# Performance work log

Measured on AMD Instinct MI355X. Metric: run time of the kernel, lower is better.

Reference implementation:

```python
import jax, jax.numpy as jnp
import numpy as np

B, S, DIM = 2, 2048, 2048
H = 16
KV_RANK = 512
D_NOPE, D_ROPE, D_V = 128, 64, 128
QK_HEAD = D_NOPE + D_ROPE  # 192
THETA = 10000.0


def make_freqs(seqlen, d_rope, theta=THETA):
    inv = 1.0 / (theta ** (np.arange(0, d_rope, 2, dtype=np.float32) / d_rope))
    ang = np.outer(np.arange(seqlen, dtype=np.float32), inv)  # [S, d/2]
    return jnp.asarray(np.cos(ang)), jnp.asarray(np.sin(ang))


def apply_rope(x, cos, sin):
    # x: [b, s, h, d]; cos/sin: [s, d//2]; complex-pair rotation (interleaved pairs)
    xr = x.reshape(*x.shape[:-1], -1, 2)
    re, im = xr[..., 0], xr[..., 1]
    c = cos[None, :, None, :]
    s = sin[None, :, None, :]
    out = jnp.stack([re * c - im * s, re * s + im * c], axis=-1)
    return out.reshape(x.shape)


def setup_inputs() -> dict:
    key = jax.random.key(0)
    ks = jax.random.split(key, 6)
    w_scale = 0.02
    cos, sin = make_freqs(S, D_ROPE)
    return {
        'x': jax.random.normal(ks[0], (B, S, DIM), dtype=jnp.float32),
        'freqs_cos': cos,
        'freqs_sin': sin,
        'wq': jax.random.normal(ks[1], (H * QK_HEAD, DIM), dtype=jnp.float32) * w_scale,
        'wkv_a': jax.random.normal(ks[2], (KV_RANK + D_ROPE, DIM), dtype=jnp.float32) * w_scale,
        'wkv_b': jax.random.normal(ks[3], (H * (D_NOPE + D_V), KV_RANK), dtype=jnp.float32) * w_scale,
        'wo': jax.random.normal(ks[4], (DIM, H * D_V), dtype=jnp.float32) * w_scale,
        'alpha': jnp.ones((1,), jnp.float32) * 0.5,
        'gamma': jnp.ones((KV_RANK,), jnp.float32),
        'beta': jnp.zeros((KV_RANK,), jnp.float32),
    }


def reference(x, freqs_cos, freqs_sin, wq, wkv_a, wkv_b, wo, alpha, gamma, beta):
    b, s, _ = x.shape
    # Q projection -> [b, s, h, qk_head]
    q = (x @ wq.T).reshape(b, s, H, QK_HEAD)
    q_nope, q_pe = q[..., :D_NOPE], q[..., D_NOPE:]
    q_pe = apply_rope(q_pe, freqs_cos, freqs_sin)

    # latent KV projection
    kv_full = x @ wkv_a.T                      # [b, s, kv_rank + d_rope]
    kv, k_pe = kv_full[..., :KV_RANK], kv_full[..., KV_RANK:]
    k_pe = apply_rope(k_pe[:, :, None, :], freqs_cos, freqs_sin)[:, :, 0, :]  # [b, s, d_rope]
    # DyT norm on latent kv
    kvn = jnp.tanh(alpha * kv) * gamma + beta  # [b, s, kv_rank]

    # absorbed attention: fold wkv_b into q and output
    wkv_b_h = wkv_b.reshape(H, D_NOPE + D_V, KV_RANK)
    wk = wkv_b_h[:, :D_NOPE]                   # [h, d_nope, c]
    wv = wkv_b_h[:, D_NOPE:]                   # [h, d_v, c]
    q_abs = jnp.einsum('bshd,hdc->bshc', q_nope, wk)  # [b, s, h, c]

    scale = QK_HEAD ** -0.5
    scores = (jnp.einsum('bshc,btc->bsht', q_abs, kvn)
              + jnp.einsum('bshr,btr->bsht', q_pe, k_pe)) * scale
    probs = jax.nn.softmax(scores, axis=-1)

    o_lat = jnp.einsum('bsht,btc->bshc', probs, kvn)          # latent-space output
    o = jnp.einsum('bshc,hdc->bshd', o_lat, wv)               # [b, s, h, d_v]
    return o.reshape(b, s, H * D_V) @ wo.T
```

## Files before the change

kernel.cpp:

```cpp
#include <hip/hip_runtime.h>
#include <math.h>

typedef __bf16 bf16x8 __attribute__((ext_vector_type(8)));
typedef float f32x4 __attribute__((ext_vector_type(4)));

#define LOG2E 1.4426950408889634f

__device__ __forceinline__ unsigned short bf16r(float f) {
  unsigned u = __float_as_uint(f);
  u = (u + 0x7fffu + ((u >> 16) & 1u)) >> 16;
  return (unsigned short)u;
}
__device__ __forceinline__ float bf2f(unsigned short h) {
  return __uint_as_float(((unsigned)h) << 16);
}

#define GLOAD16(gsrc, ldst)                                                        \
  __builtin_amdgcn_global_load_lds(                                                \
      (const __attribute__((address_space(1))) void*)(gsrc),                       \
      (__attribute__((address_space(3))) void*)(ldst), 16, 0, 0)

__device__ __forceinline__ void map_block(int& bx, int& by, int& z) {
  const int gx = gridDim.x, gy = gridDim.y;
  const int nwg = gx * gy * gridDim.z;
  int id = blockIdx.x + gx * (blockIdx.y + gy * blockIdx.z);
  if (gridDim.z == 1 && (gx & 3) == 0 && (gy & 1) == 0 && (nwg & 7) == 0) {
    const int xcd = id & 7, k = id >> 3;
    const int rx = gx >> 2, ry = gy >> 1;
    bx = (xcd & 3) * rx + (k % rx);
    by = (xcd >> 2) * ry + (k / rx);
    z = 0;
  } else {
    if ((nwg & 7) == 0) id = (id & 7) * (nwg >> 3) + (id >> 3);
    bx = id % gx;
    const int t1 = id / gx;
    by = t1 % gy;
    z = t1 / gy;
  }
}

__global__ void conv_all(const float* __restrict__ x, const float* __restrict__ wq,
                         const float* __restrict__ wkva, const float* __restrict__ wkvb,
                         const float* __restrict__ wo,
                         unsigned short* __restrict__ xb, unsigned short* __restrict__ wqb,
                         unsigned short* __restrict__ wab, unsigned short* __restrict__ wbb,
                         unsigned short* __restrict__ wob) {
  int bid = blockIdx.x;
  const float* src; unsigned short* dst; long nsrc;
  if (bid < 8192)       {               src = x;    dst = xb;  nsrc = 8388608; }
  else if (bid < 14336) { bid -= 8192;  src = wq;   dst = wqb; nsrc = 6291456; }
  else if (bid < 15616) { bid -= 14336; src = wkva; dst = wab; nsrc = 1179648; }
  else if (bid < 17664) { bid -= 15616; src = wkvb; dst = wbb; nsrc = 2097152; }
  else                  { bid -= 17664; src = wo;   dst = wob; nsrc = 4194304; }
  long i = ((long)bid * 256 + threadIdx.x) * 4;
  ushort4 o;
  if (i < nsrc) {
    float4 v = *(const float4*)&src[i];
    o.x = bf16r(v.x); o.y = bf16r(v.y); o.z = bf16r(v.z); o.w = bf16r(v.w);
  } else {
    o.x = 0; o.y = 0; o.z = 0; o.w = 0;
  }
  *(ushort4*)&dst[i] = o;
}

template <int BN, int MODE>
__global__ __launch_bounds__(512) void gemm8p(
    const unsigned short* __restrict__ A, const unsigned short* __restrict__ B,
    void* __restrict__ Cv, float* __restrict__ laux,
    int Mrows, int K, int lda, int ldb, int ldc, int zs,
    long sAh, long sAl, long sBh, long sBl, long sCh, long sCl, float alpha)
{
  constexpr int BM = 256;
  constexpr int WN = BN / 4;
  constexpr int NR = WN / 16;
  constexpr int BU = BN / 64;
  constexpr int BU1 = (BU + 1) / 2;

  __shared__ unsigned short As[2][BM * 64];
  __shared__ unsigned short Bs[2][BN * 64];

  const int tid = threadIdx.x;
  const int w = tid >> 6, l = tid & 63, lg = l & 15, lh = l >> 4;
  const int wmi = w >> 2, wni = w & 3;
  const int lrow = l >> 3;
  const int swz8 = ((l & 7) ^ lrow) * 8;

  int bx, by, z;
  map_block(bx, by, z);
  const int zh = z >> zs, zl = z & ((1 << zs) - 1);

  const unsigned short* Ab = A + zh * sAh + zl * sAl + (long)(bx * BM) * lda;
  const unsigned short* Bb = B + zh * sBh + zl * sBl + (long)(by * BN) * ldb;

  const int nt = K >> 6;

  auto stA = [&](int T, int u) {
    if (T >= nt) return;
    const int rr = u * 64 + w * 8;
    GLOAD16(Ab + (long)(rr + lrow) * lda + (T << 6) + swz8, &As[T & 1][rr * 64]);
  };
  auto stB = [&](int T, int u) {
    if (T >= nt) return;
    const int rr = u * 64 + w * 8;
    GLOAD16(Bb + (long)(rr + lrow) * ldb + (T << 6) + swz8, &Bs[T & 1][rr * 64]);
  };

  stA(0, 0); stA(0, 1); stA(0, 2); stA(0, 3);
#pragma unroll
  for (int u = 0; u < BU; ++u) stB(0, u);
  stA(1, 0); stA(1, 2);

  f32x4 acc[8][NR] = {};

  const int nit = nt >> 1;
  for (int i = 0; i < nit; ++i) {
    const int t0 = 2 * i;
#pragma unroll
    for (int j = 0; j < 8; ++j) {
      const int tau = t0 + (j >> 2);
      const int jj = j & 3;
      const int mh = jj & 1, kh = jj >> 1;
      if (jj == 0) {
        if (tau + 1 < nt) asm volatile("s_waitcnt vmcnt(2)" ::: "memory");
        else              asm volatile("s_waitcnt vmcnt(0)" ::: "memory");
      } else {
        asm volatile("" ::: "memory");
      }
      __builtin_amdgcn_s_barrier();
      if (j == 0)      { stA(t0 + 1, 1); stA(t0 + 1, 3); }
      else if (j == 1) { for (int u = 0; u < BU1; ++u) stB(t0 + 1, u); }
      else if (j == 2) { for (int u = BU1; u < BU; ++u) stB(t0 + 1, u); }
      else if (j == 3) { stA(t0 + 2, 0); stA(t0 + 2, 2); }
      else if (j == 4) { stA(t0 + 2, 1); stA(t0 + 2, 3); }
      else if (j == 5) { for (int u = 0; u < BU1; ++u) stB(t0 + 2, u); }
      else if (j == 6) { for (int u = BU1; u < BU; ++u) stB(t0 + 2, u); }
      else             { stA(t0 + 3, 0); stA(t0 + 3, 2); }
      const unsigned short* bA = As[tau & 1];
      const unsigned short* bB = Bs[tau & 1];
      const int rswz = ((kh * 4 + lh) ^ (lg & 7)) * 8;
      bf16x8 af[4], bf[NR];
#pragma unroll
      for (int mi = 0; mi < 4; ++mi)
        af[mi] = *(const bf16x8*)&bA[(wmi * 128 + mh * 64 + mi * 16 + lg) * 64 + rswz];
#pragma unroll
      for (int ni = 0; ni < NR; ++ni)
        bf[ni] = *(const bf16x8*)&bB[(wni * WN + ni * 16 + lg) * 64 + rswz];
      __builtin_amdgcn_s_setprio(1);
#pragma unroll
      for (int mi = 0; mi < 4; ++mi)
#pragma unroll
        for (int ni = 0; ni < NR; ++ni)
          acc[mh * 4 + mi][ni] = __builtin_amdgcn_mfma_f32_16x16x32_bf16(
              af[mi], bf[ni], acc[mh * 4 + mi][ni], 0, 0, 0);
      __builtin_amdgcn_s_setprio(0);
    }
  }

  if (nt & 1) {
    const int tau = nt - 1;
    asm volatile("s_waitcnt vmcnt(0)" ::: "memory");
    __builtin_amdgcn_s_barrier();
    const unsigned short* bA = As[tau & 1];
    const unsigned short* bB = Bs[tau & 1];
#pragma unroll
    for (int jj = 0; jj < 4; ++jj) {
      const int mh = jj & 1, kh = jj >> 1;
      const int rswz = ((kh * 4 + lh) ^ (lg & 7)) * 8;
      bf16x8 af[4], bf[NR];
#pragma unroll
      for (int mi = 0; mi < 4; ++mi)
        af[mi] = *(const bf16x8*)&bA[(wmi * 128 + mh * 64 + mi * 16 + lg) * 64 + rswz];
#pragma unroll
      for (int ni = 0; ni < NR; ++ni)
        bf[ni] = *(const bf16x8*)&bB[(wni * WN + ni * 16 + lg) * 64 + rswz];
      __builtin_amdgcn_s_setprio(1);
#pragma unroll
      for (int mi = 0; mi < 4; ++mi)
#pragma unroll
        for (int ni = 0; ni < NR; ++ni)
          acc[mh * 4 + mi][ni] = __builtin_amdgcn_mfma_f32_16x16x32_bf16(
              af[mi], bf[ni], acc[mh * 4 + mi][ni], 0, 0, 0);
      __builtin_amdgcn_s_setprio(0);
    }
  }

  const int row0 = bx * BM + wmi * 128;
  const int col0 = by * BN + wni * WN;
  const long coff = (long)zh * sCh + (long)zl * sCl;

  if (MODE == 4) {
#pragma unroll
    for (int mi = 0; mi < 8; ++mi)
#pragma unroll
      for (int r = 0; r < 4; ++r) {
        const int row = row0 + mi * 16 + lh * 4 + r;
        unsigned short* dq = (unsigned short*)Cv +
            (long)(row >> 11) * 6291456 + (long)by * 393216 + (long)(row & 2047) * 192;
#pragma unroll
        for (int ni = 0; ni < NR; ++ni)
          dq[wni * WN + ni * 16 + lg] = bf16r(acc[mi][ni][r] * alpha);
      }
  } else {
#pragma unroll
    for (int mi = 0; mi < 8; ++mi)
#pragma unroll
      for (int r = 0; r < 4; ++r) {
        const int row = row0 + mi * 16 + lh * 4 + r;
#pragma unroll
        for (int ni = 0; ni < NR; ++ni) {
          float v = acc[mi][ni][r] * alpha;
          if (MODE == 0)
            ((float*)Cv)[coff + (long)row * ldc + col0 + ni * 16 + lg] = v;
          else
            ((unsigned short*)Cv)[coff + (long)row * ldc + col0 + ni * 16 + lg] = bf16r(v);
        }
      }
  }
}

template <int MODE>
__global__ __launch_bounds__(256) void gemm4w(
    const unsigned short* __restrict__ A, const unsigned short* __restrict__ B,
    void* __restrict__ Cv, float* __restrict__ laux,
    int Mrows, int K, int lda, int ldb, int ldc, int zs,
    long sAh, long sAl, long sBh, long sBl, long sCh, long sCl, float alpha)
{
  constexpr int BM = 128, BN = 128, WN = 64, NR = 4;

  __shared__ unsigned short As[2][BM * 64];
  __shared__ unsigned short Bs[2][BN * 64];

  const int tid = threadIdx.x;
  const int w = tid >> 6, l = tid & 63, lg = l & 15, lh = l >> 4;
  const int wmi = w >> 1, wni = w & 1;
  const int lrow = l >> 3;
  const int swz8 = ((l & 7) ^ lrow) * 8;

  int bx, by, z;
  map_block(bx, by, z);
  const int zh = z >> zs, zl = z & ((1 << zs) - 1);

  const unsigned short* Ab = A + zh * sAh + zl * sAl + (long)(bx * BM) * lda;
  const unsigned short* Bb = B + zh * sBh + zl * sBl + (long)(by * BN) * ldb;

  const int nt = K >> 6;

  auto stage = [&](int T) {
    const int k0 = T << 6;
    const int d = T & 1;
#pragma unroll
    for (int u = 0; u < 4; ++u) {
      const int rr = u * 32 + w * 8;
      GLOAD16(Ab + (long)(rr + lrow) * lda + k0 + swz8, &As[d][rr * 64]);
    }
#pragma unroll
    for (int u = 0; u < 4; ++u) {
      const int rr = u * 32 + w * 8;
      GLOAD16(Bb + (long)(rr + lrow) * ldb + k0 + swz8, &Bs[d][rr * 64]);
    }
  };

  f32x4 acc[4][NR] = {};

  stage(0);
  for (int t = 0; t < nt; ++t) {
    asm volatile("s_waitcnt vmcnt(0)" ::: "memory");
    __builtin_amdgcn_s_barrier();
    if (t + 1 < nt) stage(t + 1);
    const unsigned short* bA = As[t & 1];
    const unsigned short* bB = Bs[t & 1];
#pragma unroll
    for (int kh = 0; kh < 2; ++kh) {
      const int rswz = ((kh * 4 + lh) ^ (lg & 7)) * 8;
      bf16x8 af[4], bf[NR];
#pragma unroll
      for (int mi = 0; mi < 4; ++mi)
        af[mi] = *(const bf16x8*)&bA[(wmi * 64 + mi * 16 + lg) * 64 + rswz];
#pragma unroll
      for (int ni = 0; ni < NR; ++ni)
        bf[ni] = *(const bf16x8*)&bB[(wni * WN + ni * 16 + lg) * 64 + rswz];
      __builtin_amdgcn_s_setprio(1);
#pragma unroll
      for (int mi = 0; mi < 4; ++mi)
#pragma unroll
        for (int ni = 0; ni < NR; ++ni)
          acc[mi][ni] = __builtin_amdgcn_mfma_f32_16x16x32_bf16(
              af[mi], bf[ni], acc[mi][ni], 0, 0, 0);
      __builtin_amdgcn_s_setprio(0);
    }
  }

  const int row0 = bx * BM + wmi * 64;
  const int col0 = by * BN + wni * WN;
  const long coff = (long)zh * sCh + (long)zl * sCl;

#pragma unroll
  for (int mi = 0; mi < 4; ++mi)
#pragma unroll
    for (int r = 0; r < 4; ++r) {
      const int row = row0 + mi * 16 + lh * 4 + r;
#pragma unroll
      for (int ni = 0; ni < NR; ++ni) {
        float v = acc[mi][ni][r] * alpha;
        if (MODE == 0)
          ((float*)Cv)[coff + (long)row * ldc + col0 + ni * 16 + lg] = v;
        else
          ((unsigned short*)Cv)[coff + (long)row * ldc + col0 + ni * 16 + lg] = bf16r(v);
      }
    }
}

__global__ __launch_bounds__(256) void attn_fused(
    const unsigned short* __restrict__ q192, const unsigned short* __restrict__ kh,
    const unsigned short* __restrict__ vhT, unsigned short* __restrict__ o_b)
{
  __shared__ unsigned short Ks[2][3 * 64 * 64];
  __shared__ unsigned short Ps[64 * 72];

  const int tid = threadIdx.x;
  const int w = tid >> 6, l = tid & 63, lg = l & 15, lh = l >> 4;
  const int wmi = w >> 1, wni = w & 1;
  const int lrow = l >> 3;
  const int swz8 = ((l & 7) ^ lrow) * 8;

  int id = blockIdx.x;
  id = (id & 7) * 128 + (id >> 3);
  const int bx = id & 31;
  const int z = id >> 5;
  const int b = z >> 4, hh = z & 15;

  const unsigned short* Qg = q192 + (long)z * 393216 + (long)(bx * 64) * 192;
  const unsigned short* Kg = kh + (long)z * 393216;
  const unsigned short* Vg = vhT + (long)z * 262144;

  bf16x8 qf[2][6];
#pragma unroll
  for (int mi = 0; mi < 2; ++mi)
#pragma unroll
    for (int s = 0; s < 6; ++s)
      qf[mi][s] = *(const bf16x8*)&Qg[(wmi * 32 + mi * 16 + lg) * 192 + s * 32 + lh * 8];

  bf16x8 ones;
#pragma unroll
  for (int j = 0; j < 8; ++j) ((unsigned short*)&ones)[j] = 0x3F80;

  auto stageK = [&](int T) {
    if (T >= 32) return;
    const unsigned short* src = Kg + (long)(T * 64) * 192;
    unsigned short* dst = Ks[T & 1];
#pragma unroll
    for (int u = 0; u < 3; ++u)
#pragma unroll
      for (int i = 0; i < 2; ++i) {
        const int rr = w * 16 + i * 8;
        GLOAD16(src + (long)(rr + lrow) * 192 + u * 64 + swz8, &dst[u * 4096 + rr * 64]);
      }
  };

  f32x4 acc_o[2][4] = {};
  f32x4 accl[2] = {};

  stageK(0);
  for (int t = 0; t < 32; ++t) {
    asm volatile("s_waitcnt vmcnt(0)" ::: "memory");
    __builtin_amdgcn_s_barrier();
    stageK(t + 1);
    const unsigned short* bK = Ks[t & 1];

    f32x4 acc_s[2][2] = {};
#pragma unroll
    for (int s = 0; s < 6; ++s) {
      const int u = s >> 1, half = s & 1;
      const int rswz = ((half * 4 + lh) ^ (lg & 7)) * 8;
      bf16x8 kf[2];
#pragma unroll
      for (int n = 0; n < 2; ++n)
        kf[n] = *(const bf16x8*)&bK[u * 4096 + (wni * 32 + n * 16 + lg) * 64 + rswz];
      __builtin_amdgcn_s_setprio(1);
#pragma unroll
      for (int mi = 0; mi < 2; ++mi)
#pragma unroll
        for (int n = 0; n < 2; ++n)
          acc_s[mi][n] = __builtin_amdgcn_mfma_f32_16x16x32_bf16(
              qf[mi][s], kf[n], acc_s[mi][n], 0, 0, 0);
      __builtin_amdgcn_s_setprio(0);
    }
#pragma unroll
    for (int mi = 0; mi < 2; ++mi)
#pragma unroll
      for (int n = 0; n < 2; ++n)
#pragma unroll
        for (int r = 0; r < 4; ++r)
          Ps[(wmi * 32 + mi * 16 + lh * 4 + r) * 72 + wni * 32 + n * 16 + lg] =
              bf16r(exp2f(acc_s[mi][n][r]));
    __builtin_amdgcn_s_barrier();

#pragma unroll
    for (int k2 = 0; k2 < 2; ++k2) {
      bf16x8 pf[2], vf[4];
#pragma unroll
      for (int mi = 0; mi < 2; ++mi)
        pf[mi] = *(const bf16x8*)&Ps[(wmi * 32 + mi * 16 + lg) * 72 + k2 * 32 + lh * 8];
#pragma unroll
      for (int n = 0; n < 4; ++n)
        vf[n] = *(const bf16x8*)&Vg[(long)(wni * 64 + n * 16 + lg) * 2048 +
                                    t * 64 + k2 * 32 + lh * 8];
      __builtin_amdgcn_s_setprio(1);
#pragma unroll
      for (int mi = 0; mi < 2; ++mi) {
        accl[mi] = __builtin_amdgcn_mfma_f32_16x16x32_bf16(pf[mi], ones, accl[mi], 0, 0, 0);
#pragma unroll
        for (int n = 0; n < 4; ++n)
          acc_o[mi][n] = __builtin_amdgcn_mfma_f32_16x16x32_bf16(
              pf[mi], vf[n], acc_o[mi][n], 0, 0, 0);
      }
      __builtin_amdgcn_s_setprio(0);
    }
  }

#pragma unroll
  for (int mi = 0; mi < 2; ++mi)
#pragma unroll
    for (int r = 0; r < 4; ++r) {
      const int row = bx * 64 + wmi * 32 + mi * 16 + lh * 4 + r;
      const float inv = 1.0f / accl[mi][r];
      unsigned short* dst = o_b + (long)(b * 2048 + row) * 2048 + hh * 128 + wni * 64;
#pragma unroll
      for (int n = 0; n < 4; ++n)
        dst[n * 16 + lg] = bf16r(acc_o[mi][n][r] * inv);
    }
}

template <int MODE>
__global__ __launch_bounds__(256) void gemm_bt2(
    const unsigned short* __restrict__ A, const unsigned short* __restrict__ B,
    void* __restrict__ Cv, float* __restrict__ laux,
    int M, int Nstore, int K, int lda, int ldb, int ldc, int zs,
    long sAh, long sAl, long sBh, long sBl, long sCh, long sCl, float alpha)
{
  __shared__ unsigned short As[128 * 32];
  __shared__ unsigned short Bs[128 * 32];
  const int tid = threadIdx.x;
  const int w = tid >> 6, l = tid & 63, lg = l & 15, lh = l >> 4;

  int bx, by, z;
  map_block(bx, by, z);

  const int zh = z >> zs, zl = z & ((1 << zs) - 1);
  const unsigned short* Ab = A + zh * sAh + zl * sAl + (long)(bx * 128) * lda;
  const unsigned short* Bb = B + zh * sBh + zl * sBl + (long)(by * 128) * ldb;
  const int srow = l >> 2;
  const int scol = (((l & 3) ^ ((l >> 3) & 3)) * 8);
  const int wm = (w >> 1) * 64, wn = (w & 1) * 64;
  f32x4 acc[4][4] = {};

  const long ra0 = (long)(w * 16 + srow) * lda + scol;
  const long ra1 = (long)(64 + w * 16 + srow) * lda + scol;
  const long rb0 = (long)(w * 16 + srow) * ldb + scol;
  const long rb1 = (long)(64 + w * 16 + srow) * ldb + scol;
  unsigned short* lA0 = &As[(w * 16) * 32];
  unsigned short* lA1 = &As[(64 + w * 16) * 32];
  unsigned short* lB0 = &Bs[(w * 16) * 32];
  unsigned short* lB1 = &Bs[(64 + w * 16) * 32];

  const int rsw = ((lh ^ ((lg >> 1) & 3)) * 8);

  for (int k0 = 0; k0 < K; k0 += 32) {
    __syncthreads();
    GLOAD16(Ab + ra0 + k0, lA0);
    GLOAD16(Ab + ra1 + k0, lA1);
    GLOAD16(Bb + rb0 + k0, lB0);
    GLOAD16(Bb + rb1 + k0, lB1);
    __syncthreads();
    bf16x8 af[4], bfr[4];
#pragma unroll
    for (int m = 0; m < 4; m++) af[m] = *(const bf16x8*)&As[(wm + m * 16 + lg) * 32 + rsw];
#pragma unroll
    for (int n = 0; n < 4; n++) bfr[n] = *(const bf16x8*)&Bs[(wn + n * 16 + lg) * 32 + rsw];
#pragma unroll
    for (int m = 0; m < 4; m++)
#pragma unroll
      for (int n = 0; n < 4; n++)
        acc[m][n] = __builtin_amdgcn_mfma_f32_16x16x32_bf16(af[m], bfr[n], acc[m][n], 0, 0, 0);
  }

  const int row0 = bx * 128 + wm, col0 = by * 128 + wn;
  long coff = zh * sCh + zl * sCl;

#pragma unroll
  for (int m = 0; m < 4; m++)
#pragma unroll
    for (int r = 0; r < 4; r++) {
      const int row = row0 + m * 16 + lh * 4 + r;
#pragma unroll
      for (int n = 0; n < 4; n++) {
        int col = col0 + n * 16 + lg;
        if (col < Nstore) {
          float v = acc[m][n][r] * alpha;
          if (MODE == 0)
            ((float*)Cv)[coff + (long)row * ldc + col] = v;
          else
            ((unsigned short*)Cv)[coff + (long)row * ldc + col] = bf16r(v);
        }
      }
    }
}

__global__ void kv_epilogue(const float* __restrict__ kvf, const float* __restrict__ fc,
                            const float* __restrict__ fs, const float* __restrict__ alpha,
                            const float* __restrict__ gamma, const float* __restrict__ beta,
                            unsigned short* __restrict__ kvn, unsigned short* __restrict__ kh) {
  const int n = blockIdx.x;
  const int b = n >> 11, s = n & 2047;
  const int tid = threadIdx.x;
  const float a = alpha[0];
  const float* src = kvf + (long)n * 576;
  unsigned short* dst = kvn + (long)n * 512;
#pragma unroll
  for (int c0 = 0; c0 < 512; c0 += 256) {
    int c = c0 + tid;
    float v = tanhf(a * src[c]) * gamma[c] + beta[c];
    dst[c] = bf16r(v);
  }
  if (tid < 32) {
    int i = tid;
    float re = src[512 + 2 * i], im = src[512 + 2 * i + 1];
    float co = fc[s * 32 + i], si = fs[s * 32 + i];
    ushort2 v;
    v.x = bf16r(re * co - im * si);
    v.y = bf16r(re * si + im * co);
#pragma unroll
    for (int h = 0; h < 16; h++)
      *(ushort2*)&kh[((long)(b * 16 + h) * 2048 + s) * 192 + 128 + 2 * i] = v;
  }
}

__global__ void q_ropefix(unsigned short* __restrict__ q192, const float* __restrict__ fc,
                          const float* __restrict__ fs) {
  const int n = blockIdx.x;
  const int b = n >> 11, s = n & 2047;
  const int tid = threadIdx.x;
  for (int it = tid; it < 512; it += 256) {
    int h = it >> 5, i = it & 31;
    unsigned short* dd = q192 + ((long)(b * 16 + h) * 2048 + s) * 192 + 128 + 2 * i;
    float re = bf2f(dd[0]), im = bf2f(dd[1]);
    float co = fc[s * 32 + i], si = fs[s * 32 + i];
    ushort2 o;
    o.x = bf16r(re * co - im * si);
    o.y = bf16r(re * si + im * co);
    *(ushort2*)dd = o;
  }
}

extern "C" void kernel_launch(void* const* d_in, const int* in_sizes, int n_in,
                              void* d_out, int out_size, void* d_ws, size_t ws_size,
                              hipStream_t stream) {
  const float* x = (const float*)d_in[0];
  const float* fc = (const float*)d_in[1];
  const float* fs = (const float*)d_in[2];
  const float* wq = (const float*)d_in[3];
  const float* wkva = (const float*)d_in[4];
  const float* wkvb = (const float*)d_in[5];
  const float* wo = (const float*)d_in[6];
  const float* alpha = (const float*)d_in[7];
  const float* gamma = (const float*)d_in[8];
  const float* beta = (const float*)d_in[9];
  float* out = (float*)d_out;

  char* p = (char*)d_ws;
  auto take = [&](size_t bytes) {
    char* r = p;
    p += (bytes + 255) & ~(size_t)255;
    return r;
  };
  unsigned short* wqb   = (unsigned short*)take(6291456ull * 2);
  float*          kvf   = (float*)take(2359296ull * 4);
  unsigned short* xb    = (unsigned short*)take(8388608ull * 2);
  unsigned short* wab   = (unsigned short*)take(1310720ull * 2);
  unsigned short* wbb   = (unsigned short*)take(2097152ull * 2);
  unsigned short* wob   = (unsigned short*)take(4194304ull * 2);
  unsigned short* kvn   = (unsigned short*)take(2097152ull * 2);
  unsigned short* kh    = (unsigned short*)take(12582912ull * 2);
  unsigned short* q192  = (unsigned short*)take(12582912ull * 2);
  unsigned short* vhT   = (unsigned short*)take(8388608ull * 2);
  unsigned short* o_b   = (unsigned short*)take(8388608ull * 2);

  const float scale = 1.0f / sqrtf(192.0f);
  const float scaleL = scale * LOG2E;

  conv_all<<<21760, 256, 0, stream>>>(x, wq, wkva, wkvb, wo, xb, wqb, wab, wbb, wob);

  gemm8p<192, 4><<<dim3(16, 16, 1), 512, 0, stream>>>(
      xb, wqb, q192, nullptr, 4096, 2048, 2048, 2048, 192, 0, 0, 0, 0, 0, 0, 0, scaleL);
  gemm_bt2<0><<<dim3(32, 5, 1), 256, 0, stream>>>(xb, wab, kvf, nullptr, 4096, 576, 2048,
                                                  2048, 2048, 576, 0, 0, 0, 0, 0, 0, 0, 1.0f);
  kv_epilogue<<<4096, 256, 0, stream>>>(kvf, fc, fs, alpha, gamma, beta, kvn, kh);
  gemm4w<1><<<dim3(16, 1, 32), 256, 0, stream>>>(
      kvn, wbb, kh, nullptr, 2048, 512, 512, 512, 192, 4,
      1048576, 0, 0, 131072, 6291456, 393216, 1.0f);
  q_ropefix<<<4096, 256, 0, stream>>>(q192, fc, fs);
  gemm4w<1><<<dim3(1, 16, 32), 256, 0, stream>>>(
      wbb + 128 * 512, kvn, vhT, nullptr, 128, 512, 512, 512, 2048, 4,
      0, 131072, 1048576, 0, 4194304, 262144, 1.0f);

  attn_fused<<<1024, 256, 0, stream>>>(q192, kh, vhT, o_b);

  gemm4w<0><<<dim3(32, 16, 1), 256, 0, stream>>>(
      o_b, wob, out, nullptr, 4096, 2048, 2048, 2048, 2048, 0,
      0, 0, 0, 0, 0, 0, 1.0f);
}
```

Measured before the change: 389.2 us.

## Prefetch V fragments one tile ahead in attention and batch K LDS reads

The attention kernel now loads the next tile's V fragments into registers during the current tile, using double-buffered register arrays and a loop unrolled by two, so global V latency overlaps the QK and softmax work. K fragment LDS reads are grouped per 64-column chunk, and launch bounds request two blocks per CU. The LOG2E factor moves from the Q projection scale into the exp, and the bf16 conversion uses the hardware cast. Holding sixteen extra bf16x8 registers per thread may raise register pressure or cause spills under the occupancy hint.

```diff
diff --git a/kernel.cpp b/kernel.cpp
--- a/kernel.cpp
+++ b/kernel.cpp
@@ -10,6 +10,10 @@
   unsigned u = __float_as_uint(f);
   u = (u + 0x7fffu + ((u >> 16) & 1u)) >> 16;
   return (unsigned short)u;
+}
+__device__ __forceinline__ unsigned short bfc(float f) {
+  __bf16 h = (__bf16)f;
+  return __builtin_bit_cast(unsigned short, h);
 }
 __device__ __forceinline__ float bf2f(unsigned short h) {
   return __uint_as_float(((unsigned)h) << 16);
@@ -310,7 +314,7 @@
     }
 }
 
-__global__ __launch_bounds__(256) void attn_fused(
+__global__ __launch_bounds__(256, 2) void attn_fused(
     const unsigned short* __restrict__ q192, const unsigned short* __restrict__ kh,
     const unsigned short* __restrict__ vhT, unsigned short* __restrict__ o_b)
 {
@@ -356,33 +360,49 @@
         GLOAD16(src + (long)(rr + lrow) * 192 + u * 64 + swz8, &dst[u * 4096 + rr * 64]);
       }
   };
+  auto loadV = [&](int T, bf16x8 (&vf)[8]) {
+    if (T >= 32) return;
+#pragma unroll
+    for (int j = 0; j < 8; ++j)
+      vf[j] = *(const bf16x8*)&Vg[(long)(wni * 64 + (j & 3) * 16 + lg) * 2048 +
+                                  T * 64 + (j >> 2) * 32 + lh * 8];
+  };
 
   f32x4 acc_o[2][4] = {};
   f32x4 accl[2] = {};
+  bf16x8 vfA[8], vfB[8];
 
   stageK(0);
-  for (int t = 0; t < 32; ++t) {
+  loadV(0, vfA);
+
+  auto tile = [&](int t, bf16x8 (&vcur)[8], bf16x8 (&vnext)[8]) {
     asm volatile("s_waitcnt vmcnt(0)" ::: "memory");
     __builtin_amdgcn_s_barrier();
     stageK(t + 1);
+    loadV(t + 1, vnext);
     const unsigned short* bK = Ks[t & 1];
 
     f32x4 acc_s[2][2] = {};
 #pragma unroll
-    for (int s = 0; s < 6; ++s) {
-      const int u = s >> 1, half = s & 1;
-      const int rswz = ((half * 4 + lh) ^ (lg & 7)) * 8;
-      bf16x8 kf[2];
-#pragma unroll
-      for (int n = 0; n < 2; ++n)
-        kf[n] = *(const bf16x8*)&bK[u * 4096 + (wni * 32 + n * 16 + lg) * 64 + rswz];
+    for (int u = 0; u < 3; ++u) {
+      bf16x8 kf[4];
+#pragma unroll
+      for (int half = 0; half < 2; ++half) {
+        const int rswz = ((half * 4 + lh) ^ (lg & 7)) * 8;
+#pragma unroll
+        for (int n = 0; n < 2; ++n)
+          kf[half * 2 + n] =
+              *(const bf16x8*)&bK[u * 4096 + (wni * 32 + n * 16 + lg) * 64 + rswz];
+      }
       __builtin_amdgcn_s_setprio(1);
 #pragma unroll
-      for (int mi = 0; mi < 2; ++mi)
-#pragma unroll
-        for (int n = 0; n < 2; ++n)
-          acc_s[mi][n] = __builtin_amdgcn_mfma_f32_16x16x32_bf16(
-              qf[mi][s], kf[n], acc_s[mi][n], 0, 0, 0);
+      for (int half = 0; half < 2; ++half)
+#pragma unroll
+        for (int mi = 0; mi < 2; ++mi)
+#pragma unroll
+          for (int n = 0; n < 2; ++n)
+            acc_s[mi][n] = __builtin_amdgcn_mfma_f32_16x16x32_bf16(
+                qf[mi][u * 2 + half], kf[half * 2 + n], acc_s[mi][n], 0, 0, 0);
       __builtin_amdgcn_s_setprio(0);
     }
 #pragma unroll
@@ -392,19 +412,15 @@
 #pragma unroll
         for (int r = 0; r < 4; ++r)
           Ps[(wmi * 32 + mi * 16 + lh * 4 + r) * 72 + wni * 32 + n * 16 + lg] =
-              bf16r(exp2f(acc_s[mi][n][r]));
+              bfc(exp2f(acc_s[mi][n][r] * LOG2E));
     __builtin_amdgcn_s_barrier();
 
 #pragma unroll
     for (int k2 = 0; k2 < 2; ++k2) {
-      bf16x8 pf[2], vf[4];
+      bf16x8 pf[2];
 #pragma unroll
       for (int mi = 0; mi < 2; ++mi)
         pf[mi] = *(const bf16x8*)&Ps[(wmi * 32 + mi * 16 + lg) * 72 + k2 * 32 + lh * 8];
-#pragma unroll
-      for (int n = 0; n < 4; ++n)
-        vf[n] = *(const bf16x8*)&Vg[(long)(wni * 64 + n * 16 + lg) * 2048 +
-                                    t * 64 + k2 * 32 + lh * 8];
       __builtin_amdgcn_s_setprio(1);
 #pragma unroll
       for (int mi = 0; mi < 2; ++mi) {
@@ -412,10 +428,15 @@
 #pragma unroll
         for (int n = 0; n < 4; ++n)
           acc_o[mi][n] = __builtin_amdgcn_mfma_f32_16x16x32_bf16(
-              pf[mi], vf[n], acc_o[mi][n], 0, 0, 0);
+              pf[mi], vcur[k2 * 4 + n], acc_o[mi][n], 0, 0, 0);
       }
       __builtin_amdgcn_s_setprio(0);
     }
+  };
+
+  for (int tt = 0; tt < 16; ++tt) {
+    tile(2 * tt, vfA, vfB);
+    tile(2 * tt + 1, vfB, vfA);
   }
 
 #pragma unroll
@@ -427,7 +448,7 @@
       unsigned short* dst = o_b + (long)(b * 2048 + row) * 2048 + hh * 128 + wni * 64;
 #pragma unroll
       for (int n = 0; n < 4; ++n)
-        dst[n * 16 + lg] = bf16r(acc_o[mi][n][r] * inv);
+        dst[n * 16 + lg] = bfc(acc_o[mi][n][r] * inv);
     }
 }
 
@@ -586,12 +607,11 @@
   unsigned short* o_b   = (unsigned short*)take(8388608ull * 2);
 
   const float scale = 1.0f / sqrtf(192.0f);
-  const float scaleL = scale * LOG2E;
 
   conv_all<<<21760, 256, 0, stream>>>(x, wq, wkva, wkvb, wo, xb, wqb, wab, wbb, wob);
 
   gemm8p<192, 4><<<dim3(16, 16, 1), 512, 0, stream>>>(
-      xb, wqb, q192, nullptr, 4096, 2048, 2048, 2048, 192, 0, 0, 0, 0, 0, 0, 0, scaleL);
+      xb, wqb, q192, nullptr, 4096, 2048, 2048, 2048, 192, 0, 0, 0, 0, 0, 0, 0, scale);
   gemm_bt2<0><<<dim3(32, 5, 1), 256, 0, stream>>>(xb, wab, kvf, nullptr, 4096, 576, 2048,
                                                   2048, 2048, 576, 0, 0, 0, 0, 0, 0, 0, 1.0f);
   kv_epilogue<<<4096, 256, 0, stream>>>(kvf, fc, fs, alpha, gamma, beta, kvn, kh);
```

Measured after the change: 369.1 us. 5.2% less time.
